# Performance work log

Measured on AMD Instinct MI355X. Metric: run time of the kernel, lower is better.

Reference implementation:

```python
import jax, jax.numpy as jnp
import numpy as np

BS, SEQ, DIM = 4, 2048, 1024
N_EXPERTS = 8


def setup_inputs() -> dict:
    key = jax.random.key(0)
    k_x, k_w, k_i = jax.random.split(key, 3)
    X = jax.random.normal(k_x, (BS, SEQ, DIM), dtype=jnp.float32)
    # trunc_normal init with std = in_features ** -0.5 (plain normal is fine for a reference)
    W = jax.random.normal(k_w, (N_EXPERTS, DIM, DIM), dtype=jnp.float32) * (DIM ** -0.5)
    indices = jax.random.randint(k_i, (BS, SEQ), 0, N_EXPERTS, dtype=jnp.int32)
    return {"X": X, "W": W, "indices": indices}


def reference(X, W, indices):
    # Y[b, s, :] = X[b, s, :] @ W[indices[b, s]].T   (F.linear semantics)
    # Dense per-expert matmuls + masked accumulate: avoids gathering a
    # [bs, seq, out, in] weight tensor; loop is over the small fixed expert count.
    n = W.shape[0]
    Y = jnp.zeros(X.shape[:2] + (W.shape[1],), dtype=X.dtype)
    for e in range(n):
        mask = (indices == e)[..., None]                      # [bs, seq, 1]
        Ye = jnp.einsum('bsd,od->bso', X, W[e])               # [bs, seq, out]
        Y = jnp.where(mask, Ye, Y)
    return Y
```

## Files before the change

### kernel.cpp

```cpp
#include <hip/hip_runtime.h>
#include <stdint.h>

#define T_TOK 8192
#define DIMK 1024
#define NEXP 8
#define BM 128
#define BN 128
#define BK 64
#define NTK (DIMK / BK)
#define MAXROWS (T_TOK + NEXP * BM)
#define MAXTILES (T_TOK / BM + NEXP)
#define NT (DIMK / BN)
#define NWG (MAXTILES * NT)

typedef __attribute__((ext_vector_type(4))) float f32x4;
typedef __attribute__((ext_vector_type(8))) short short8;
typedef __attribute__((ext_vector_type(8))) unsigned short us8;

__device__ __forceinline__ unsigned short f2bf(float f) {
  uint32_t u = __builtin_bit_cast(uint32_t, f);
  u += 0x7FFFu + ((u >> 16) & 1u);
  return (unsigned short)(u >> 16);
}

__device__ __forceinline__ void gload_lds16(const void* g, void* l) {
  __builtin_amdgcn_global_load_lds(
      (const __attribute__((address_space(1))) void*)g,
      (__attribute__((address_space(3))) void*)l, 16, 0, 0);
}

__global__ void k_prep_conv(const int* __restrict__ idx, const float* __restrict__ W,
                            const float* __restrict__ X, int* __restrict__ hdr,
                            int* __restrict__ row2tok, unsigned short* __restrict__ Wb,
                            unsigned short* __restrict__ Xb) {
  const int tid = threadIdx.x;
  const int b = blockIdx.x;
  if (b == 0) {
    __shared__ int h[NEXP];
    __shared__ int cur[NEXP];
    __shared__ int segs[NEXP + 1];
    if (tid < NEXP) h[tid] = 0;
    __syncthreads();
    for (int i = tid; i < T_TOK; i += 256) atomicAdd(&h[idx[i]], 1);
    __syncthreads();
    if (tid == 0) {
      int off = 0;
      for (int e = 0; e < NEXP; e++) {
        segs[e] = off; cur[e] = off;
        hdr[e] = h[e]; hdr[8 + e] = off;
        off += ((h[e] + BM - 1) >> 7) << 7;
      }
      segs[NEXP] = off;
    }
    __syncthreads();
    for (int e = 0; e < NEXP; e++)
      for (int p = segs[e] + h[e] + tid; p < segs[e + 1]; p += 256) row2tok[p] = -1;
    for (int p = segs[NEXP] + tid; p < MAXROWS; p += 256) row2tok[p] = -1;
    for (int i = tid; i < T_TOK; i += 256) {
      int e = idx[i];
      int pos = atomicAdd(&cur[e], 1);
      row2tok[pos] = i;
    }
    return;
  }
  const float* src;
  unsigned short* dst;
  if (b <= 4096) {
    size_t base = (size_t)(b - 1) * 2048 + tid * 8;
    src = W + base; dst = Wb + base;
  } else {
    size_t base = (size_t)(b - 4097) * 2048 + tid * 8;
    src = X + base; dst = Xb + base;
  }
  f32x4 v0 = *(const f32x4*)src;
  f32x4 v1 = *(const f32x4*)(src + 4);
  us8 o;
  o[0] = f2bf(v0[0]); o[1] = f2bf(v0[1]); o[2] = f2bf(v0[2]); o[3] = f2bf(v0[3]);
  o[4] = f2bf(v1[0]); o[5] = f2bf(v1[1]); o[6] = f2bf(v1[2]); o[7] = f2bf(v1[3]);
  *(us8*)dst = o;
}

__global__ __launch_bounds__(512, 6) void k_gemm(
    const unsigned short* __restrict__ Xb, const unsigned short* __restrict__ Wb,
    const int* __restrict__ hdr, const int* __restrict__ row2tok,
    float* __restrict__ out) {
  __shared__ unsigned short A_lds[BM * BK];
  __shared__ unsigned short B_lds[BN * BK];

  int T[NEXP];
#pragma unroll
  for (int i = 0; i < NEXP; i++) T[i] = (hdr[i] + BM - 1) >> 7;

  const int orig = blockIdx.x;
  const int xcd = orig & 7;
  const int slot = orig >> 3;
  int e = -1, tl = 0, nq = 0;
  {
    int P = T[xcd] < 9 ? T[xcd] : 9;
    if (slot < 8 * P) {
      e = xcd; tl = slot % P; nq = slot / P;
    } else {
      int r = slot - 8 * P;
      for (int i = 0; i < xcd; i++) r += 72 - 8 * (T[i] < 9 ? T[i] : 9);
      for (int i = 0; i < NEXP && e < 0; i++) {
        int ot = T[i] - 9;
        if (ot > 0) {
          if (r < 8 * ot) { e = i; tl = 9 + r % ot; nq = r / ot; }
          else r -= 8 * ot;
        }
      }
    }
  }
  if (e < 0) return;
  const int n0 = nq * BN;
  const int row0 = hdr[8 + e] + tl * BM;

  const int tid = threadIdx.x;
  const int lane = tid & 63;
  const int wid = tid >> 6;
  const int wr = wid >> 2, wc = wid & 3;

  const int st_r = lane >> 3;
  const int st_cb = ((lane & 7) ^ st_r) << 4;

  const char* a_lane_base[2];
#pragma unroll
  for (int j = 0; j < 2; j++) {
    int r = (wid * 2 + j) * 8 + st_r;
    int tok = row2tok[row0 + r];
    if (tok < 0) tok = 0;
    a_lane_base[j] = (const char*)Xb + (size_t)tok * (DIMK * 2) + st_cb;
  }
  const char* b_base = (const char*)Wb + ((size_t)e * DIMK * DIMK + (size_t)n0 * DIMK) * 2;

  f32x4 acc[4][2];
  const f32x4 fzero = {0.f, 0.f, 0.f, 0.f};
#pragma unroll
  for (int m = 0; m < 4; m++)
#pragma unroll
    for (int n = 0; n < 2; n++) acc[m][n] = fzero;

  const int rsel = lane & 15;
  const int swz_r = (lane & 7) << 4;
  const int kgrp = (lane >> 4) << 4;

  int a_row_b[4], b_row_b[2];
#pragma unroll
  for (int m = 0; m < 4; m++) a_row_b[m] = (wr * 64 + m * 16 + rsel) * (BK * 2);
#pragma unroll
  for (int n = 0; n < 2; n++) b_row_b[n] = (wc * 32 + n * 16 + rsel) * (BK * 2);

  for (int kt = 0; kt < NTK; kt++) {
    const int k0b = kt * (BK * 2);
#pragma unroll
    for (int j = 0; j < 2; j++) {
      int c = wid * 2 + j;
      int r = c * 8 + st_r;
      gload_lds16(a_lane_base[j] + k0b, (char*)A_lds + c * 1024);
      gload_lds16(b_base + (size_t)r * (DIMK * 2) + k0b + st_cb, (char*)B_lds + c * 1024);
    }
    __syncthreads();
#pragma unroll
    for (int ks = 0; ks < 2; ks++) {
      const int kb = ks * 64 + kgrp;
      short8 av[4], bv[2];
#pragma unroll
      for (int m = 0; m < 4; m++)
        av[m] = *(const short8*)((const char*)A_lds + a_row_b[m] + (kb ^ swz_r));
#pragma unroll
      for (int n = 0; n < 2; n++)
        bv[n] = *(const short8*)((const char*)B_lds + b_row_b[n] + (kb ^ swz_r));
#pragma unroll
      for (int m = 0; m < 4; m++)
#pragma unroll
        for (int n = 0; n < 2; n++)
          acc[m][n] = __builtin_amdgcn_mfma_f32_16x16x32_bf16(av[m], bv[n], acc[m][n], 0, 0, 0);
    }
    __syncthreads();
  }

  const int rg4 = (lane >> 4) * 4;
#pragma unroll
  for (int m = 0; m < 4; m++) {
#pragma unroll
    for (int i = 0; i < 4; i++) {
      int rg = row0 + wr * 64 + m * 16 + rg4 + i;
      int tok = row2tok[rg];
      if (tok >= 0) {
        float* po = out + (size_t)tok * DIMK + n0 + wc * 32 + rsel;
#pragma unroll
        for (int n = 0; n < 2; n++) po[n * 16] = acc[m][n][i];
      }
    }
  }
}

extern "C" void kernel_launch(void* const* d_in, const int* in_sizes, int n_in,
                              void* d_out, int out_size, void* d_ws, size_t ws_size,
                              hipStream_t stream) {
  const float* X = (const float*)d_in[0];
  const float* W = (const float*)d_in[1];
  const int* idx = (const int*)d_in[2];
  float* out = (float*)d_out;
  char* ws = (char*)d_ws;

  int* hdr = (int*)ws;
  int* row2tok = (int*)(ws + 256);
  unsigned short* Wb = (unsigned short*)(ws + 65536);
  unsigned short* Xb = (unsigned short*)(ws + 65536 + 16777216);

  k_prep_conv<<<8193, 256, 0, stream>>>(idx, W, X, hdr, row2tok, Wb, Xb);
  k_gemm<<<NWG, 512, 0, stream>>>(Xb, Wb, hdr, row2tok, out);
}
```

Before: 59.73 us.

## Double-buffer A tile in LDS and prefetch B through registers

Double-buffers the A tile in LDS using async global-to-LDS loads for the next k-step, and prefetches the B tile into registers before computing, then writes it to LDS after a barrier. This overlaps global memory latency with the MFMA work on the current tile. It lowers the launch-bounds occupancy hint from 6 to 4 to allow more registers. In exchange it adds a second barrier per iteration and uses more LDS and registers, which may reduce the number of resident workgroups.

```diff
diff --git a/kernel.cpp b/kernel.cpp
--- a/kernel.cpp
+++ b/kernel.cpp
@@ -80,11 +80,11 @@
   *(us8*)dst = o;
 }
 
-__global__ __launch_bounds__(512, 6) void k_gemm(
+__global__ __launch_bounds__(512, 4) void k_gemm(
     const unsigned short* __restrict__ Xb, const unsigned short* __restrict__ Wb,
     const int* __restrict__ hdr, const int* __restrict__ row2tok,
     float* __restrict__ out) {
-  __shared__ unsigned short A_lds[BM * BK];
+  __shared__ unsigned short A_lds[2][BM * BK];
   __shared__ unsigned short B_lds[BN * BK];
 
   int T[NEXP];
@@ -132,6 +132,15 @@
     a_lane_base[j] = (const char*)Xb + (size_t)tok * (DIMK * 2) + st_cb;
   }
   const char* b_base = (const char*)Wb + ((size_t)e * DIMK * DIMK + (size_t)n0 * DIMK) * 2;
+  const char* b_src[2];
+  char* b_dst[2];
+#pragma unroll
+  for (int j = 0; j < 2; j++) {
+    int c = wid * 2 + j;
+    int r = c * 8 + st_r;
+    b_src[j] = b_base + (size_t)r * (DIMK * 2) + st_cb;
+    b_dst[j] = (char*)B_lds + c * 1024 + lane * 16;
+  }
 
   f32x4 acc[4][2];
   const f32x4 fzero = {0.f, 0.f, 0.f, 0.f};
@@ -150,23 +159,35 @@
 #pragma unroll
   for (int n = 0; n < 2; n++) b_row_b[n] = (wc * 32 + n * 16 + rsel) * (BK * 2);
 
+  short8 breg[2];
+#pragma unroll
+  for (int j = 0; j < 2; j++)
+    gload_lds16(a_lane_base[j], (char*)A_lds[0] + (wid * 2 + j) * 1024);
+#pragma unroll
+  for (int j = 0; j < 2; j++) breg[j] = *(const short8*)(b_src[j]);
+  __syncthreads();
+#pragma unroll
+  for (int j = 0; j < 2; j++) *(short8*)(b_dst[j]) = breg[j];
+  __syncthreads();
+
+  int cur = 0;
+#pragma unroll 1
   for (int kt = 0; kt < NTK; kt++) {
-    const int k0b = kt * (BK * 2);
-#pragma unroll
-    for (int j = 0; j < 2; j++) {
-      int c = wid * 2 + j;
-      int r = c * 8 + st_r;
-      gload_lds16(a_lane_base[j] + k0b, (char*)A_lds + c * 1024);
-      gload_lds16(b_base + (size_t)r * (DIMK * 2) + k0b + st_cb, (char*)B_lds + c * 1024);
-    }
-    __syncthreads();
+    if (kt + 1 < NTK) {
+      const int k0b = (kt + 1) * (BK * 2);
+#pragma unroll
+      for (int j = 0; j < 2; j++)
+        gload_lds16(a_lane_base[j] + k0b, (char*)A_lds[cur ^ 1] + (wid * 2 + j) * 1024);
+#pragma unroll
+      for (int j = 0; j < 2; j++) breg[j] = *(const short8*)(b_src[j] + k0b);
+    }
 #pragma unroll
     for (int ks = 0; ks < 2; ks++) {
       const int kb = ks * 64 + kgrp;
       short8 av[4], bv[2];
 #pragma unroll
       for (int m = 0; m < 4; m++)
-        av[m] = *(const short8*)((const char*)A_lds + a_row_b[m] + (kb ^ swz_r));
+        av[m] = *(const short8*)((const char*)A_lds[cur] + a_row_b[m] + (kb ^ swz_r));
 #pragma unroll
       for (int n = 0; n < 2; n++)
         bv[n] = *(const short8*)((const char*)B_lds + b_row_b[n] + (kb ^ swz_r));
@@ -177,6 +198,12 @@
           acc[m][n] = __builtin_amdgcn_mfma_f32_16x16x32_bf16(av[m], bv[n], acc[m][n], 0, 0, 0);
     }
     __syncthreads();
+    if (kt + 1 < NTK) {
+#pragma unroll
+      for (int j = 0; j < 2; j++) *(short8*)(b_dst[j]) = breg[j];
+    }
+    __syncthreads();
+    cur ^= 1;
   }
 
   const int rg4 = (lane >> 4) * 4;
```

Result: slower. 62.67 us (+4.9%).
